# Performance work log

Measured on AMD Instinct MI355X. Metric: run time of the kernel, lower is better.

## Reference

```python
import jax, jax.numpy as jnp
import numpy as np

INV_TEMP = 20.0
THRESHOLD = 0.01
SING_CUTOFF = 3.0
D0 = 128  # order-0 descriptor block
EPS = 1e-6


def setup_inputs() -> dict:
    key = jax.random.key(0)
    ks = jax.random.split(key, 6)
    B, N, M, D = 4, 4096, 4096, 256
    K = (D - D0) // 2
    return {
        "keypoints_A": jax.random.uniform(ks[0], (B, N, 2), jnp.float32) * 2.0 - 1.0,
        "descriptions_A": jax.random.normal(ks[1], (B, N, D), jnp.float32),
        "keypoints_B": jax.random.uniform(ks[2], (B, M, 2), jnp.float32) * 2.0 - 1.0,
        "descriptions_B": jax.random.normal(ks[3], (B, M, D), jnp.float32),
        "W_lstsq": jax.random.normal(ks[4], (D0, K), jnp.float32) * 0.1,
        "b_lstsq": jnp.zeros((K,), jnp.float32),
    }


def _svdvals_2x2(A):
    # singular values of [..,2,2] via eigenvalues of A^T A (closed form)
    M = jnp.einsum('...ki,...kj->...ij', A, A)
    t = M[..., 0, 0] + M[..., 1, 1]
    d = M[..., 0, 0] * M[..., 1, 1] - M[..., 0, 1] * M[..., 1, 0]
    disc = jnp.sqrt(jnp.maximum(0.25 * t * t - d, 0.0))
    lam_hi = 0.5 * t + disc
    lam_lo = jnp.maximum(0.5 * t - disc, 0.0)
    return jnp.sqrt(lam_hi), jnp.sqrt(lam_lo)


def reference(keypoints_A, descriptions_A, keypoints_B, descriptions_B, W_lstsq, b_lstsq):
    B, N, D = descriptions_A.shape
    K = (D - D0) // 2
    # --- dual softmax matcher (normalize=True) ---
    dA = descriptions_A / jnp.linalg.norm(descriptions_A, axis=-1, keepdims=True)
    dB = descriptions_B / jnp.linalg.norm(descriptions_B, axis=-1, keepdims=True)
    sim = INV_TEMP * jnp.einsum('bnd,bmd->bnm', dA, dB)  # [B,N,M]
    P = jax.nn.softmax(sim, axis=-2) * jax.nn.softmax(sim, axis=-1)
    # --- mutual nearest neighbors, fixed-shape (one candidate per A-row) ---
    j = jnp.argmax(P, axis=-1)  # [B,N]
    Pij = jnp.take_along_axis(P, j[..., None], axis=-1)[..., 0]
    colmax_j = jnp.take_along_axis(P.max(axis=-2), j, axis=-1)
    valid = (Pij >= colmax_j) & (Pij > THRESHOLD)  # mutual max + threshold
    # --- gather raw descriptors for matched pairs ---
    descB_m = jnp.take_along_axis(descriptions_B, j[..., None], axis=1)  # [B,N,D]
    desc0_A, desc1_A = descriptions_A[..., :D0], descriptions_A[..., D0:]
    desc0_B, desc1_B = descB_m[..., :D0], descB_m[..., D0:]
    # --- lstsq weights from order-0 features ---
    wA = jax.nn.softplus(desc0_A @ W_lstsq + b_lstsq)
    wB = jax.nn.softplus(desc0_B @ W_lstsq + b_lstsq)
    w = jnp.sqrt(wA * wB)  # [B,N,K]
    # --- weighted 2x2 affine lstsq: A x ~ y ---
    X = desc1_A.reshape(B, N, K, 2)
    Y = desc1_B.reshape(B, N, K, 2)
    G = jnp.einsum('bnk,bnki,bnkj->bnij', w, X, X) + EPS * jnp.eye(2, dtype=X.dtype)
    C = jnp.einsum('bnk,bnki,bnkj->bnij', w, Y, X)
    est = jnp.swapaxes(jnp.linalg.solve(G, jnp.swapaxes(C, -1, -2)), -1, -2)  # [B,N,2,2]
    # --- singular value / determinant filter ---
    s_hi, s_lo = _svdvals_2x2(est)
    good = jnp.isfinite(s_hi + s_lo) & (s_hi < SING_CUTOFF) & (s_lo > 1.0 / SING_CUTOFF)
    det = est[..., 0, 0] * est[..., 1, 1] - est[..., 0, 1] * est[..., 1, 0]
    good = good & (det > 0)  # remove_negative_determinants=True
    valid = valid & good
    matches_A = keypoints_A  # row i of A pairs with column j[b,i]
    matches_B = jnp.take_along_axis(keypoints_B, j[..., None], axis=1)
    return matches_A, matches_B, j, valid
```

## Files before the change

kernel.cpp:

```cpp
#include <hip/hip_runtime.h>
#include <math.h>

#define Bb   4
#define Nn   4096
#define Mm   4096
#define Dd   256
#define D0c  128
#define Kc   64

typedef _Float16 half8 __attribute__((ext_vector_type(8)));
typedef float    f32x4 __attribute__((ext_vector_type(4)));

__device__ __forceinline__ unsigned encf(float f) {
    unsigned u = __float_as_uint(f);
    return (u & 0x80000000u) ? ~u : (u | 0x80000000u);
}
__device__ __forceinline__ float decf(unsigned u) {
    return (u & 0x80000000u) ? __uint_as_float(u ^ 0x80000000u) : __uint_as_float(~u);
}
__device__ __forceinline__ float softplusf(float x) {
    return fmaxf(x, 0.f) + log1pf(expf(-fabsf(x)));
}
__device__ __forceinline__ void gl_lds16(const _Float16* g, _Float16* l) {
    __builtin_amdgcn_global_load_lds((const __attribute__((address_space(1))) void*)g,
                                     (__attribute__((address_space(3))) void*)l, 16, 0, 0);
}

__device__ __forceinline__ void decode_tile(int bid, int swz, int& mt, int& nt, int& zz) {
    if (swz == 2) {
        const int xcd = bid & 7, k = bid >> 3;
        zz = xcd >> 2;
        const int s = xcd & 3;
        mt = (s & 1) * 16 + (k & 15);
        nt = (s >> 1) * 16 + (k >> 4);
    } else if (swz == 1) {
        const int xcd = bid & 7, k = bid >> 3;
        zz = 0;
        const int s = xcd >> 1;
        const int t = (xcd & 1) * 128 + k;
        mt = (s & 1) * 16 + (t & 15);
        nt = (s >> 1) * 16 + (t >> 4);
    } else {
        mt = bid & 31; nt = (bid >> 5) & 31; zz = bid >> 10;
    }
}

__global__ __launch_bounds__(256) void prep_kernel(
    const float* __restrict__ dA, const float* __restrict__ dB,
    _Float16* __restrict__ Ah, _Float16* __restrict__ Al,
    _Float16* __restrict__ Bh, _Float16* __restrict__ Bl,
    unsigned* __restrict__ colMaxU)
{
    const int t = threadIdx.x, wave = t >> 6, lane = t & 63;
    const int row = blockIdx.x * 4 + wave;
    if (blockIdx.y == 0 && lane == 0) colMaxU[row] = 0u;
    const float* src = blockIdx.y ? dB : dA;
    _Float16* dh = blockIdx.y ? Bh : Ah;
    _Float16* dl = blockIdx.y ? Bl : Al;
    const float4 v = *(const float4*)&src[(size_t)row * Dd + lane * 4];
    float ss = v.x * v.x + v.y * v.y + v.z * v.z + v.w * v.w;
#pragma unroll
    for (int m = 32; m; m >>= 1) ss += __shfl_xor(ss, m, 64);
    const float inv = 1.0f / sqrtf(ss);
    float x[4] = {v.x * inv, v.y * inv, v.z * inv, v.w * inv};
    union { _Float16 h[4]; uint2 u; } ph, pl;
#pragma unroll
    for (int i = 0; i < 4; i++) {
        _Float16 h = (_Float16)x[i];
        ph.h[i] = h;
        pl.h[i] = (_Float16)(x[i] - (float)h);
    }
    const size_t toff = (size_t)(row >> 7) * 32768
                      + (size_t)(lane >> 3) * 4096
                      + (size_t)((lane >> 1) & 3) * 1024
                      + (size_t)(row & 127) * 8 + (lane & 1) * 4;
    *(uint2*)&dh[toff] = ph.u;
    *(uint2*)&dl[toff] = pl.u;
}

template<int PB, int STORE>
__global__ __launch_bounds__(256, 3) void sim_kernel(
    const _Float16* __restrict__ Ah, const _Float16* __restrict__ Al,
    const _Float16* __restrict__ Bh, const _Float16* __restrict__ Bl,
    const float* __restrict__ Lrow_g, const float* __restrict__ Lcol_g,
    float* __restrict__ rowsumP, float* __restrict__ colsumP,
    float* __restrict__ rkey, int* __restrict__ rmArr, float* __restrict__ rcvArr,
    unsigned* __restrict__ cmU, float* __restrict__ simG, int b0, int swz)
{
    __shared__ _Float16 lds[4][4][128][8];
    __shared__ float    colp[128];
    __shared__ float    rowp[128];
    __shared__ unsigned colu[128];
    __shared__ float    shL[128], shLc[128];
    __shared__ float    s_bk[128], s_bc[128];
    __shared__ int      s_bm[128];

    const int t = threadIdx.x;
    const int wave = t >> 6, lane = t & 63;
    const int wr = wave >> 1, wc = wave & 1;
    int mt, nt, bbl;
    decode_tile(blockIdx.x, swz, mt, nt, bbl);
    const int bb = b0 + bbl;
    const int n0 = nt * 128, m0 = mt * 128;

    if (PB) {
        if (t < 128) {
            shL[t]  = Lrow_g[bb * Nn + n0 + t];
            shLc[t] = Lcol_g[bb * Mm + m0 + t];
            colu[t] = 0u;
        }
    } else {
        if (t < 128) { colp[t] = 0.f; rowp[t] = 0.f; }
    }

    const _Float16* gb;
    {
        const size_t offA = (size_t)(bb * Nn + n0) * Dd;
        const size_t offB = (size_t)(bb * Mm + m0) * Dd;
        if      (wave == 0) gb = Ah + offA;
        else if (wave == 1) gb = Al + offA;
        else if (wave == 2) gb = Bh + offB;
        else                gb = Bl + offB;
    }

    f32x4 acc[4][4];
#pragma unroll
    for (int ti = 0; ti < 4; ti++)
#pragma unroll
        for (int tj = 0; tj < 4; tj++) acc[ti][tj] = (f32x4)0.f;

    const int quad = lane >> 4, l15 = lane & 15;
    _Float16* ldsw = &lds[wave][0][0][0];

    for (int kc8 = 0; kc8 < 8; ++kc8) {
        const _Float16* gsrc = gb + kc8 * 4096;
#pragma unroll
        for (int q = 0; q < 8; ++q)
            gl_lds16(gsrc + q * 512 + lane * 8, ldsw + q * 512);
        __syncthreads();

        half8 afh[4], afl[4];
#pragma unroll
        for (int ti = 0; ti < 4; ++ti) {
            afh[ti] = *(const half8*)&lds[0][quad][wr * 64 + ti * 16 + l15][0];
            afl[ti] = *(const half8*)&lds[1][quad][wr * 64 + ti * 16 + l15][0];
        }
#pragma unroll
        for (int tj = 0; tj < 4; ++tj) {
            half8 bh = *(const half8*)&lds[2][quad][wc * 64 + tj * 16 + l15][0];
            half8 bl = *(const half8*)&lds[3][quad][wc * 64 + tj * 16 + l15][0];
#pragma unroll
            for (int ti = 0; ti < 4; ++ti) {
                acc[ti][tj] = __builtin_amdgcn_mfma_f32_16x16x32_f16(afh[ti], bh, acc[ti][tj], 0, 0, 0);
                acc[ti][tj] = __builtin_amdgcn_mfma_f32_16x16x32_f16(afh[ti], bl, acc[ti][tj], 0, 0, 0);
                acc[ti][tj] = __builtin_amdgcn_mfma_f32_16x16x32_f16(afl[ti], bh, acc[ti][tj], 0, 0, 0);
            }
        }
        __syncthreads();
    }

    if (!PB) {
        float rp[16] = {0.f}, cp[4] = {0.f};
#pragma unroll
        for (int ti = 0; ti < 4; ++ti)
#pragma unroll
            for (int tj = 0; tj < 4; ++tj)
#pragma unroll
                for (int r = 0; r < 4; ++r) {
                    float e = __expf(fmaf(20.f, acc[ti][tj][r], -20.f));
                    rp[ti * 4 + r] += e;
                    cp[tj] += e;
                }
#pragma unroll
        for (int i = 0; i < 16; ++i)
#pragma unroll
            for (int m = 1; m < 16; m <<= 1) rp[i] += __shfl_xor(rp[i], m, 64);
        if (l15 == 0) {
#pragma unroll
            for (int ti = 0; ti < 4; ++ti)
#pragma unroll
                for (int r = 0; r < 4; ++r)
                    atomicAdd(&rowp[wr * 64 + ti * 16 + quad * 4 + r], rp[ti * 4 + r]);
        }
#pragma unroll
        for (int tj = 0; tj < 4; ++tj) {
            cp[tj] += __shfl_xor(cp[tj], 16, 64);
            cp[tj] += __shfl_xor(cp[tj], 32, 64);
        }
        if (quad == 0) {
#pragma unroll
            for (int tj = 0; tj < 4; ++tj) atomicAdd(&colp[wc * 64 + tj * 16 + l15], cp[tj]);
        }
        __syncthreads();
        if (t < 128) {
            rowsumP[(size_t)(bb * 32 + mt) * Nn + n0 + t] = rowp[t];
            colsumP[(size_t)(bb * 32 + nt) * Mm + m0 + t] = colp[t];
        }
        if (STORE) {
            float* base = simG + ((size_t)bbl * Nn + n0) * Mm + m0 + wc * 64;
#pragma unroll
            for (int ti = 0; ti < 4; ++ti)
#pragma unroll
                for (int r = 0; r < 4; ++r) {
                    float* rowp_ = base + (size_t)(wr * 64 + ti * 16 + quad * 4 + r) * Mm;
#pragma unroll
                    for (int tj = 0; tj < 4; ++tj)
                        __builtin_nontemporal_store(acc[ti][tj][r], rowp_ + tj * 16 + l15);
                }
        }
    } else {
        float Lr[16];
#pragma unroll
        for (int ti = 0; ti < 4; ++ti)
#pragma unroll
            for (int r = 0; r < 4; ++r)
                Lr[ti * 4 + r] = shL[wr * 64 + ti * 16 + quad * 4 + r];

        float bk[16], bc[16];
        int bm[16];
        unsigned cu[4];
#pragma unroll
        for (int i = 0; i < 16; i++) { bk[i] = -INFINITY; bc[i] = -INFINITY; bm[i] = 0x7fffffff; }
#pragma unroll
        for (int j = 0; j < 4; j++) cu[j] = 0u;

#pragma unroll
        for (int ti = 0; ti < 4; ++ti)
#pragma unroll
            for (int tj = 0; tj < 4; ++tj)
#pragma unroll
                for (int r = 0; r < 4; ++r) {
                    float cv = fmaf(40.f, acc[ti][tj][r], -40.f - Lr[ti * 4 + r]);
                    float kv = cv - shLc[wc * 64 + tj * 16 + l15];
                    const int i = ti * 4 + r;
                    if (kv > bk[i]) { bk[i] = kv; bm[i] = m0 + wc * 64 + tj * 16 + l15; bc[i] = cv; }
                    unsigned e = encf(cv);
                    if (e > cu[tj]) cu[tj] = e;
                }
#pragma unroll
        for (int i = 0; i < 16; ++i) {
#pragma unroll
            for (int m = 1; m < 16; m <<= 1) {
                float okv = __shfl_xor(bk[i], m, 64);
                int   om  = __shfl_xor(bm[i], m, 64);
                float ocv = __shfl_xor(bc[i], m, 64);
                if (okv > bk[i] || (okv == bk[i] && om < bm[i])) { bk[i] = okv; bm[i] = om; bc[i] = ocv; }
            }
        }
        if (l15 == 0 && wc == 0) {
#pragma unroll
            for (int ti = 0; ti < 4; ++ti)
#pragma unroll
                for (int r = 0; r < 4; ++r) {
                    const int row = wr * 64 + ti * 16 + quad * 4 + r, i = ti * 4 + r;
                    s_bk[row] = bk[i]; s_bm[row] = bm[i]; s_bc[row] = bc[i];
                }
        }
        __syncthreads();
        if (l15 == 0 && wc == 1) {
#pragma unroll
            for (int ti = 0; ti < 4; ++ti)
#pragma unroll
                for (int r = 0; r < 4; ++r) {
                    const int row = wr * 64 + ti * 16 + quad * 4 + r, i = ti * 4 + r;
                    float k0 = s_bk[row];
                    if (bk[i] > k0 || (bk[i] == k0 && bm[i] < s_bm[row])) {
                        s_bk[row] = bk[i]; s_bm[row] = bm[i]; s_bc[row] = bc[i];
                    }
                }
        }
#pragma unroll
        for (int tj = 0; tj < 4; ++tj) {
            unsigned o = __shfl_xor(cu[tj], 16, 64); if (o > cu[tj]) cu[tj] = o;
            o = __shfl_xor(cu[tj], 32, 64); if (o > cu[tj]) cu[tj] = o;
        }
        if (quad == 0) {
#pragma unroll
            for (int tj = 0; tj < 4; ++tj) atomicMax(&colu[wc * 64 + tj * 16 + l15], cu[tj]);
        }
        __syncthreads();
        if (t < 128) {
            size_t idx = (size_t)(bb * 32 + mt) * Nn + n0 + t;
            rkey[idx] = s_bk[t]; rmArr[idx] = s_bm[t]; rcvArr[idx] = s_bc[t];
            cmU[(size_t)(bb * 32 + nt) * Mm + m0 + t] = colu[t];
        }
    }
}

__global__ __launch_bounds__(256) void logsum_kernel(
    const float* __restrict__ rowsumP, const float* __restrict__ colsumP,
    float* __restrict__ Lrow, float* __restrict__ Lcol, int b0, int CB)
{
    int t = blockIdx.x * 256 + threadIdx.x;
    int half = CB * 4096;
    int which = t >= half;
    int idx = which ? (t - half) : t;
    int bb = b0 + (idx >> 12), n = idx & 4095;
    const float* P = which ? colsumP : rowsumP;
    float s = 0.f;
    for (int mt = 0; mt < 32; ++mt) s += P[(size_t)(bb * 32 + mt) * 4096 + n];
    (which ? Lcol : Lrow)[bb * 4096 + n] = logf(s);
}

__global__ __launch_bounds__(256) void scan_kernel(
    const float* __restrict__ simG,
    const float* __restrict__ Lrow, const float* __restrict__ Lcol,
    float* __restrict__ kvP, float* __restrict__ cvP, int* __restrict__ jP,
    unsigned* __restrict__ colMaxU, int b0)
{
    __shared__ unsigned colu[1024];
    const int t = threadIdx.x, wave = t >> 6, lane = t & 63;
    const int blk = blockIdx.x;
    const int bbl = blk >> 10;
    const int r10 = blk & 1023;
    const int stripe = r10 >> 2, q = r10 & 3;
    const int bb = b0 + bbl;
    const int col0 = q * 1024;
    const int row0 = stripe * 16 + wave * 4;

    for (int i = t; i < 1024; i += 256) colu[i] = 0u;
    __syncthreads();

    f32x4 Lc4[4], cmax[4];
    const float* LcB = Lcol + bb * Mm + col0;
#pragma unroll
    for (int c = 0; c < 4; ++c) {
        Lc4[c] = *(const f32x4*)&LcB[c * 256 + lane * 4];
        cmax[c] = (f32x4)(-INFINITY);
    }

    const float* rowbase = simG + (size_t)(bbl * Nn + row0) * Mm + col0;
    f32x4 cur[4], nxt[4];
#pragma unroll
    for (int c = 0; c < 4; ++c)
        cur[c] = __builtin_nontemporal_load((const f32x4*)&rowbase[c * 256 + lane * 4]);

    for (int r = 0; r < 4; ++r) {
        if (r < 3) {
            const float* nrow = rowbase + (size_t)(r + 1) * Mm;
#pragma unroll
            for (int c = 0; c < 4; ++c)
                nxt[c] = __builtin_nontemporal_load((const f32x4*)&nrow[c * 256 + lane * 4]);
        }
        const int n = bb * Nn + row0 + r;
        const float Ln = Lrow[n];
        const float cbias = -40.f - Ln;
        float bk = -INFINITY, bc = -INFINITY;
        int bm = 0x7fffffff;
#pragma unroll
        for (int c = 0; c < 4; ++c) {
            float cv0 = fmaf(40.f, cur[c].x, cbias);
            float cv1 = fmaf(40.f, cur[c].y, cbias);
            float cv2 = fmaf(40.f, cur[c].z, cbias);
            float cv3 = fmaf(40.f, cur[c].w, cbias);
            cmax[c].x = fmaxf(cmax[c].x, cv0);
            cmax[c].y = fmaxf(cmax[c].y, cv1);
            cmax[c].z = fmaxf(cmax[c].z, cv2);
            cmax[c].w = fmaxf(cmax[c].w, cv3);
            const int mb = col0 + c * 256 + lane * 4;
            float kv0 = cv0 - Lc4[c].x;
            float kv1 = cv1 - Lc4[c].y;
            float kv2 = cv2 - Lc4[c].z;
            float kv3 = cv3 - Lc4[c].w;
            if (kv0 > bk) { bk = kv0; bm = mb;     bc = cv0; }
            if (kv1 > bk) { bk = kv1; bm = mb + 1; bc = cv1; }
            if (kv2 > bk) { bk = kv2; bm = mb + 2; bc = cv2; }
            if (kv3 > bk) { bk = kv3; bm = mb + 3; bc = cv3; }
        }
#pragma unroll
        for (int sh = 1; sh < 64; sh <<= 1) {
            float okv = __shfl_xor(bk, sh, 64);
            int   om  = __shfl_xor(bm, sh, 64);
            float ocv = __shfl_xor(bc, sh, 64);
            if (okv > bk || (okv == bk && om < bm)) { bk = okv; bm = om; bc = ocv; }
        }
        if (lane == 0) {
            size_t o = ((size_t)bb * Nn + row0 + r) * 4 + q;
            kvP[o] = bk; cvP[o] = bc; jP[o] = bm;
        }
#pragma unroll
        for (int c = 0; c < 4; ++c) cur[c] = nxt[c];
    }
#pragma unroll
    for (int c = 0; c < 4; ++c) {
        const int mb = c * 256 + lane * 4;
        atomicMax(&colu[mb],     encf(cmax[c].x));
        atomicMax(&colu[mb + 1], encf(cmax[c].y));
        atomicMax(&colu[mb + 2], encf(cmax[c].z));
        atomicMax(&colu[mb + 3], encf(cmax[c].w));
    }
    __syncthreads();
    unsigned* cm = colMaxU + (size_t)bb * Mm + col0;
    for (int i = t; i < 1024; i += 256) atomicMax(&cm[i], colu[i]);
}

__global__ __launch_bounds__(256) void validate_kernel(
    const float* __restrict__ kvP, const float* __restrict__ cvP,
    const int* __restrict__ jP, const unsigned* __restrict__ colMaxU,
    float* __restrict__ outJ, int* __restrict__ jIdx, int* __restrict__ v1)
{
    const float LOG_THR = -4.605170185988091f;
    const int p = blockIdx.x * 256 + threadIdx.x;
    const int bb = p >> 12;
    float bk = -INFINITY, bc = -INFINITY;
    int bm = 0x7fffffff;
#pragma unroll
    for (int q = 0; q < 4; ++q) {
        size_t o = (size_t)p * 4 + q;
        float k = kvP[o];
        int   m = jP[o];
        if (k > bk || (k == bk && m < bm)) { bk = k; bm = m; bc = cvP[o]; }
    }
    const float cm = decf(colMaxU[(size_t)bb * Mm + bm]);
    const int ok = (bk > LOG_THR) && (bc >= cm);
    outJ[p] = (float)bm;
    jIdx[p] = bm;
    v1[p] = ok;
}

__global__ __launch_bounds__(256) void finalize_kernel(
    const float* __restrict__ rkey, const int* __restrict__ rmArr,
    const float* __restrict__ rcvArr, const unsigned* __restrict__ cmU,
    float* __restrict__ outJ, int* __restrict__ jIdx, int* __restrict__ v1)
{
    const float LOG_THR = -4.605170185988091f;
    int p = blockIdx.x * 256 + threadIdx.x;
    int bb = p >> 12, n = p & 4095;
    float bk = -INFINITY, bc = -INFINITY;
    int bm = 0;
    for (int mt = 0; mt < 32; ++mt) {
        size_t idx = (size_t)(bb * 32 + mt) * Nn + n;
        float k = rkey[idx];
        if (k > bk) { bk = k; bm = rmArr[idx]; bc = rcvArr[idx]; }
    }
    unsigned u = 0u;
    for (int nt = 0; nt < 32; ++nt) {
        unsigned c = cmU[(size_t)(bb * 32 + nt) * Mm + bm];
        if (c > u) u = c;
    }
    float cm = decf(u);
    int ok = (bk > LOG_THR) && (bc >= cm);
    outJ[p] = (float)bm;
    jIdx[p] = bm;
    v1[p]   = ok;
}

__global__ __launch_bounds__(256) void affine_kernel(
    const float* __restrict__ descA, const float* __restrict__ descB,
    const float* __restrict__ kpA, const float* __restrict__ kpB,
    const float* __restrict__ W, const float* __restrict__ bvec,
    const int* __restrict__ jIdx, const int* __restrict__ v1,
    float* __restrict__ outA, float* __restrict__ outB, float* __restrict__ outV)
{
    __shared__ float Ws[D0c * Kc];
    __shared__ float sbuf[4][4][D0c];
    const int t = threadIdx.x, wave = t >> 6, lane = t & 63;
    for (int i = t; i < D0c * Kc; i += 256) Ws[i] = W[i];
    const float bl = bvec[lane];
    __syncthreads();

    float* s0A = sbuf[wave][0];
    float* s1A = sbuf[wave][1];
    float* s0B = sbuf[wave][2];
    float* s1B = sbuf[wave][3];

    for (int p = 0; p < 8; ++p) {
        const int point = blockIdx.x * 32 + wave * 8 + p;
        const int bb = point >> 12;
        const int j = jIdx[point];
        const float* da = descA + (size_t)point * Dd;
        const float* db = descB + (size_t)(bb * Mm + j) * Dd;
        s0A[lane] = da[lane];       s0A[64 + lane] = da[64 + lane];
        s1A[lane] = da[128 + lane]; s1A[64 + lane] = da[192 + lane];
        s0B[lane] = db[lane];       s0B[64 + lane] = db[64 + lane];
        s1B[lane] = db[128 + lane]; s1B[64 + lane] = db[192 + lane];
        __syncthreads();

        float xa = bl, xb = bl;
#pragma unroll 8
        for (int d = 0; d < 128; ++d) {
            float w_ = Ws[d * 64 + lane];
            xa = fmaf(s0A[d], w_, xa);
            xb = fmaf(s0B[d], w_, xb);
        }
        float wa = softplusf(xa), wb = softplusf(xb);
        float w = sqrtf(wa * wb);
        float x0 = s1A[2 * lane], x1 = s1A[2 * lane + 1];
        float y0 = s1B[2 * lane], y1 = s1B[2 * lane + 1];
        float g00 = w * x0 * x0, g01 = w * x0 * x1, g11 = w * x1 * x1;
        float c00 = w * y0 * x0, c01 = w * y0 * x1;
        float c10 = w * y1 * x0, c11 = w * y1 * x1;
#pragma unroll
        for (int m = 32; m; m >>= 1) {
            g00 += __shfl_xor(g00, m, 64); g01 += __shfl_xor(g01, m, 64); g11 += __shfl_xor(g11, m, 64);
            c00 += __shfl_xor(c00, m, 64); c01 += __shfl_xor(c01, m, 64);
            c10 += __shfl_xor(c10, m, 64); c11 += __shfl_xor(c11, m, 64);
        }
        if (lane == 0) {
            g00 += 1e-6f; g11 += 1e-6f;
            float det = g00 * g11 - g01 * g01;
            float e00 = (c00 * g11 - c01 * g01) / det;
            float e01 = (c01 * g00 - c00 * g01) / det;
            float e10 = (c10 * g11 - c11 * g01) / det;
            float e11 = (c11 * g00 - c10 * g01) / det;
            float m00 = e00 * e00 + e10 * e10;
            float m01 = e00 * e01 + e10 * e11;
            float m11 = e01 * e01 + e11 * e11;
            float tr = m00 + m11;
            float dm = m00 * m11 - m01 * m01;
            float disc = sqrtf(fmaxf(0.25f * tr * tr - dm, 0.f));
            float lhi = 0.5f * tr + disc;
            float llo = fmaxf(0.5f * tr - disc, 0.f);
            float shi = sqrtf(lhi), slo = sqrtf(llo);
            float sdet = e00 * e11 - e01 * e10;
            int good = isfinite(shi + slo) && (shi < 3.0f) && (slo > 0.33333334f) && (sdet > 0.f);
            int valid = v1[point] && good;
            outA[2 * point]     = kpA[2 * point];
            outA[2 * point + 1] = kpA[2 * point + 1];
            const float* kb = kpB + (size_t)(bb * Mm + j) * 2;
            outB[2 * point]     = kb[0];
            outB[2 * point + 1] = kb[1];
            outV[point] = valid ? 1.f : 0.f;
        }
        __syncthreads();
    }
}

extern "C" void kernel_launch(void* const* d_in, const int* in_sizes, int n_in,
                              void* d_out, int out_size, void* d_ws, size_t ws_size,
                              hipStream_t stream) {
    const float* kpA = (const float*)d_in[0];
    const float* dA  = (const float*)d_in[1];
    const float* kpB = (const float*)d_in[2];
    const float* dB  = (const float*)d_in[3];
    const float* W   = (const float*)d_in[4];
    const float* bl  = (const float*)d_in[5];
    float* out = (float*)d_out;

    char* ws = (char*)d_ws;
    _Float16* Ah = (_Float16*)ws;  ws += 8388608;
    _Float16* Al = (_Float16*)ws;  ws += 8388608;
    _Float16* Bh = (_Float16*)ws;  ws += 8388608;
    _Float16* Bl = (_Float16*)ws;  ws += 8388608;
    float*    rowsumP = (float*)ws;    ws += 2097152;
    float*    colsumP = (float*)ws;    ws += 2097152;
    float*    Lrow    = (float*)ws;    ws += 65536;
    float*    Lcol    = (float*)ws;    ws += 65536;
    int*      jIdx    = (int*)ws;      ws += 65536;
    int*      v1      = (int*)ws;      ws += 65536;
    float*    kvP     = (float*)ws;    ws += 262144;
    float*    cvP     = (float*)ws;    ws += 262144;
    int*      jP      = (int*)ws;      ws += 262144;
    unsigned* colMaxU = (unsigned*)ws; ws += 65536;
    char*     big     = ws;

    const size_t base = (size_t)(big - (char*)d_ws);

    float*    rkey  = (float*)big;
    int*      rmArr = (int*)(big + 2097152);
    float*    rcvArr= (float*)(big + 4194304);
    unsigned* cmU   = (unsigned*)(big + 6291456);

    float* outA = out;
    float* outB = out + 32768;
    float* outJ = out + 65536;
    float* outV = out + 81920;

    const size_t per = 67108864ull;
    int CB = 0;
    if      (ws_size >= base + 2 * per) CB = 2;
    else if (ws_size >= base + 1 * per) CB = 1;

    prep_kernel<<<dim3(4096, 2), 256, 0, stream>>>(dA, dB, Ah, Al, Bh, Bl, colMaxU);

    if (CB) {
        float* simG = (float*)big;
        for (int b0 = 0; b0 < Bb; b0 += CB) {
            sim_kernel<0, 1><<<1024 * CB, 256, 0, stream>>>(
                Ah, Al, Bh, Bl, nullptr, nullptr, rowsumP, colsumP,
                nullptr, nullptr, nullptr, nullptr, simG, b0, CB);
            logsum_kernel<<<32 * CB, 256, 0, stream>>>(rowsumP, colsumP, Lrow, Lcol, b0, CB);
            scan_kernel<<<1024 * CB, 256, 0, stream>>>(simG, Lrow, Lcol, kvP, cvP, jP, colMaxU, b0);
        }
        validate_kernel<<<64, 256, 0, stream>>>(kvP, cvP, jP, colMaxU, outJ, jIdx, v1);
    } else {
        sim_kernel<0, 0><<<4096, 256, 0, stream>>>(
            Ah, Al, Bh, Bl, nullptr, nullptr, rowsumP, colsumP,
            nullptr, nullptr, nullptr, nullptr, nullptr, 0, 0);
        logsum_kernel<<<32 * Bb, 256, 0, stream>>>(rowsumP, colsumP, Lrow, Lcol, 0, Bb);
        sim_kernel<1, 0><<<4096, 256, 0, stream>>>(
            Ah, Al, Bh, Bl, Lrow, Lcol, nullptr, nullptr,
            rkey, rmArr, rcvArr, cmU, nullptr, 0, 0);
        finalize_kernel<<<64, 256, 0, stream>>>(rkey, rmArr, rcvArr, cmU, outJ, jIdx, v1);
    }
    affine_kernel<<<512, 256, 0, stream>>>(dA, dB, kpA, kpB, W, bl, jIdx, v1, outA, outB, outV);
}
```

Baseline: 304.1 us.

## Fuse previous batch's row/column scan into next batch's similarity GEMM

Replaces the two-batch chunked pipeline with per-batch double-buffered similarity buffers. While computing batch b's similarity tile, two waves of each block scan batch b-1's stored similarity rows, producing row argmax keys and column maxima. Only the last batch gets a standalone scan. The aim is to hide the memory-bound scan behind MFMA work and remove separate scan launches. The cost is extra register pressure and extra load traffic inside the GEMM kernel, plus a dependence on the block-to-stripe mapping.

```diff
diff --git a/kernel.cpp b/kernel.cpp
--- a/kernel.cpp
+++ b/kernel.cpp
@@ -27,13 +27,7 @@
 }
 
 __device__ __forceinline__ void decode_tile(int bid, int swz, int& mt, int& nt, int& zz) {
-    if (swz == 2) {
-        const int xcd = bid & 7, k = bid >> 3;
-        zz = xcd >> 2;
-        const int s = xcd & 3;
-        mt = (s & 1) * 16 + (k & 15);
-        nt = (s >> 1) * 16 + (k >> 4);
-    } else if (swz == 1) {
+    if (swz == 1) {
         const int xcd = bid & 7, k = bid >> 3;
         zz = 0;
         const int s = xcd >> 1;
@@ -78,14 +72,15 @@
     *(uint2*)&dl[toff] = pl.u;
 }
 
-template<int PB, int STORE>
+template<int PB, int STORE, int SCAN>
 __global__ __launch_bounds__(256, 3) void sim_kernel(
     const _Float16* __restrict__ Ah, const _Float16* __restrict__ Al,
     const _Float16* __restrict__ Bh, const _Float16* __restrict__ Bl,
     const float* __restrict__ Lrow_g, const float* __restrict__ Lcol_g,
     float* __restrict__ rowsumP, float* __restrict__ colsumP,
     float* __restrict__ rkey, int* __restrict__ rmArr, float* __restrict__ rcvArr,
-    unsigned* __restrict__ cmU, float* __restrict__ simG, int b0, int swz)
+    unsigned* __restrict__ cmU, float* __restrict__ simG,
+    const float* __restrict__ simPrev, int b0, int swz)
 {
     __shared__ _Float16 lds[4][4][128][8];
     __shared__ float    colp[128];
@@ -94,6 +89,7 @@
     __shared__ float    shL[128], shLc[128];
     __shared__ float    s_bk[128], s_bc[128];
     __shared__ int      s_bm[128];
+    __shared__ float    shLp[16];
 
     const int t = threadIdx.x;
     const int wave = t >> 6, lane = t & 63;
@@ -111,6 +107,21 @@
         }
     } else {
         if (t < 128) { colp[t] = 0.f; rowp[t] = 0.f; }
+    }
+
+    int stripe_s = 0, q_s = 0;
+    f32x4 Lc4s[4], cmaxs[4];
+    if (SCAN) {
+        stripe_s = blockIdx.x >> 2;
+        q_s = blockIdx.x & 3;
+        if (t < 16) shLp[t] = Lrow_g[(size_t)(b0 - 1) * Nn + stripe_s * 16 + t];
+        if (wave < 2) {
+            const float* LcB = Lcol_g + (size_t)(b0 - 1) * Mm + q_s * 1024;
+#pragma unroll
+            for (int c = 0; c < 4; ++c) Lc4s[c] = *(const f32x4*)&LcB[c * 256 + lane * 4];
+        }
+#pragma unroll
+        for (int c = 0; c < 4; ++c) cmaxs[c] = (f32x4)(-INFINITY);
     }
 
     const _Float16* gb;
@@ -133,6 +144,14 @@
     _Float16* ldsw = &lds[wave][0][0][0];
 
     for (int kc8 = 0; kc8 < 8; ++kc8) {
+        f32x4 curs[4];
+        if (SCAN && wave < 2) {
+            const int rr = kc8 * 2 + wave;
+            const float* rp = simPrev + (size_t)(stripe_s * 16 + rr) * Mm + q_s * 1024;
+#pragma unroll
+            for (int c = 0; c < 4; ++c)
+                curs[c] = __builtin_nontemporal_load((const f32x4*)&rp[c * 256 + lane * 4]);
+        }
         const _Float16* gsrc = gb + kc8 * 4096;
 #pragma unroll
         for (int q = 0; q < 8; ++q)
@@ -156,6 +175,44 @@
                 acc[ti][tj] = __builtin_amdgcn_mfma_f32_16x16x32_f16(afl[ti], bh, acc[ti][tj], 0, 0, 0);
             }
         }
+        if (SCAN && wave < 2) {
+            const int rr = kc8 * 2 + wave;
+            const float Ln = shLp[rr];
+            const float cbias = -40.f - Ln;
+            float bk = -INFINITY, bc = -INFINITY;
+            int bm = 0x7fffffff;
+#pragma unroll
+            for (int c = 0; c < 4; ++c) {
+                float cv0 = fmaf(40.f, curs[c].x, cbias);
+                float cv1 = fmaf(40.f, curs[c].y, cbias);
+                float cv2 = fmaf(40.f, curs[c].z, cbias);
+                float cv3 = fmaf(40.f, curs[c].w, cbias);
+                cmaxs[c].x = fmaxf(cmaxs[c].x, cv0);
+                cmaxs[c].y = fmaxf(cmaxs[c].y, cv1);
+                cmaxs[c].z = fmaxf(cmaxs[c].z, cv2);
+                cmaxs[c].w = fmaxf(cmaxs[c].w, cv3);
+                const int mb = q_s * 1024 + c * 256 + lane * 4;
+                float kv0 = cv0 - Lc4s[c].x;
+                float kv1 = cv1 - Lc4s[c].y;
+                float kv2 = cv2 - Lc4s[c].z;
+                float kv3 = cv3 - Lc4s[c].w;
+                if (kv0 > bk) { bk = kv0; bm = mb;     bc = cv0; }
+                if (kv1 > bk) { bk = kv1; bm = mb + 1; bc = cv1; }
+                if (kv2 > bk) { bk = kv2; bm = mb + 2; bc = cv2; }
+                if (kv3 > bk) { bk = kv3; bm = mb + 3; bc = cv3; }
+            }
+#pragma unroll
+            for (int sh = 1; sh < 64; sh <<= 1) {
+                float okv = __shfl_xor(bk, sh, 64);
+                int   om  = __shfl_xor(bm, sh, 64);
+                float ocv = __shfl_xor(bc, sh, 64);
+                if (okv > bk || (okv == bk && om < bm)) { bk = okv; bm = om; bc = ocv; }
+            }
+            if (lane == 0) {
+                size_t o = ((size_t)(b0 - 1) * Nn + stripe_s * 16 + rr) * 4 + q_s;
+                rkey[o] = bk; rcvArr[o] = bc; rmArr[o] = bm;
+            }
+        }
         __syncthreads();
     }
 
@@ -207,6 +264,25 @@
                     for (int tj = 0; tj < 4; ++tj)
                         __builtin_nontemporal_store(acc[ti][tj][r], rowp_ + tj * 16 + l15);
                 }
+        }
+        if (SCAN) {
+            unsigned* colu2 = (unsigned*)&lds[0][0][0][0];
+            __syncthreads();
+            for (int i = t; i < 1024; i += 256) colu2[i] = 0u;
+            __syncthreads();
+            if (wave < 2) {
+#pragma unroll
+                for (int c = 0; c < 4; ++c) {
+                    const int mb = c * 256 + lane * 4;
+                    atomicMax(&colu2[mb],     encf(cmaxs[c].x));
+                    atomicMax(&colu2[mb + 1], encf(cmaxs[c].y));
+                    atomicMax(&colu2[mb + 2], encf(cmaxs[c].z));
+                    atomicMax(&colu2[mb + 3], encf(cmaxs[c].w));
+                }
+            }
+            __syncthreads();
+            unsigned* cm = cmU + (size_t)(b0 - 1) * Mm + q_s * 1024;
+            for (int i = t; i < 1024; i += 256) atomicMax(&cm[i], colu2[i]);
         }
     } else {
         float Lr[16];
@@ -311,10 +387,8 @@
     __shared__ unsigned colu[1024];
     const int t = threadIdx.x, wave = t >> 6, lane = t & 63;
     const int blk = blockIdx.x;
-    const int bbl = blk >> 10;
-    const int r10 = blk & 1023;
-    const int stripe = r10 >> 2, q = r10 & 3;
-    const int bb = b0 + bbl;
+    const int stripe = blk >> 2, q = blk & 3;
+    const int bb = b0;
     const int col0 = q * 1024;
     const int row0 = stripe * 16 + wave * 4;
 
@@ -322,14 +396,14 @@
     __syncthreads();
 
     f32x4 Lc4[4], cmax[4];
-    const float* LcB = Lcol + bb * Mm + col0;
+    const float* LcB = Lcol + (size_t)bb * Mm + col0;
 #pragma unroll
     for (int c = 0; c < 4; ++c) {
         Lc4[c] = *(const f32x4*)&LcB[c * 256 + lane * 4];
         cmax[c] = (f32x4)(-INFINITY);
     }
 
-    const float* rowbase = simG + (size_t)(bbl * Nn + row0) * Mm + col0;
+    const float* rowbase = simG + (size_t)row0 * Mm + col0;
     f32x4 cur[4], nxt[4];
 #pragma unroll
     for (int c = 0; c < 4; ++c)
@@ -342,8 +416,7 @@
             for (int c = 0; c < 4; ++c)
                 nxt[c] = __builtin_nontemporal_load((const f32x4*)&nrow[c * 256 + lane * 4]);
         }
-        const int n = bb * Nn + row0 + r;
-        const float Ln = Lrow[n];
+        const float Ln = Lrow[(size_t)bb * Nn + row0 + r];
         const float cbias = -40.f - Ln;
         float bk = -INFINITY, bc = -INFINITY;
         int bm = 0x7fffffff;
@@ -567,30 +640,36 @@
     float* outV = out + 81920;
 
     const size_t per = 67108864ull;
-    int CB = 0;
-    if      (ws_size >= base + 2 * per) CB = 2;
-    else if (ws_size >= base + 1 * per) CB = 1;
+    const int havebuf = (ws_size >= base + 2 * per);
 
     prep_kernel<<<dim3(4096, 2), 256, 0, stream>>>(dA, dB, Ah, Al, Bh, Bl, colMaxU);
 
-    if (CB) {
-        float* simG = (float*)big;
-        for (int b0 = 0; b0 < Bb; b0 += CB) {
-            sim_kernel<0, 1><<<1024 * CB, 256, 0, stream>>>(
-                Ah, Al, Bh, Bl, nullptr, nullptr, rowsumP, colsumP,
-                nullptr, nullptr, nullptr, nullptr, simG, b0, CB);
-            logsum_kernel<<<32 * CB, 256, 0, stream>>>(rowsumP, colsumP, Lrow, Lcol, b0, CB);
-            scan_kernel<<<1024 * CB, 256, 0, stream>>>(simG, Lrow, Lcol, kvP, cvP, jP, colMaxU, b0);
-        }
+    if (havebuf) {
+        float* buf0 = (float*)big;
+        float* buf1 = (float*)(big + per);
+        for (int bb = 0; bb < Bb; ++bb) {
+            float*       cur  = (bb & 1) ? buf1 : buf0;
+            const float* prev = (bb & 1) ? buf0 : buf1;
+            if (bb == 0)
+                sim_kernel<0, 1, 0><<<1024, 256, 0, stream>>>(
+                    Ah, Al, Bh, Bl, nullptr, nullptr, rowsumP, colsumP,
+                    nullptr, nullptr, nullptr, nullptr, cur, nullptr, bb, 1);
+            else
+                sim_kernel<0, 1, 1><<<1024, 256, 0, stream>>>(
+                    Ah, Al, Bh, Bl, Lrow, Lcol, rowsumP, colsumP,
+                    kvP, jP, cvP, colMaxU, cur, prev, bb, 1);
+            logsum_kernel<<<32, 256, 0, stream>>>(rowsumP, colsumP, Lrow, Lcol, bb, 1);
+        }
+        scan_kernel<<<1024, 256, 0, stream>>>(buf1, Lrow, Lcol, kvP, cvP, jP, colMaxU, 3);
         validate_kernel<<<64, 256, 0, stream>>>(kvP, cvP, jP, colMaxU, outJ, jIdx, v1);
     } else {
-        sim_kernel<0, 0><<<4096, 256, 0, stream>>>(
+        sim_kernel<0, 0, 0><<<4096, 256, 0, stream>>>(
             Ah, Al, Bh, Bl, nullptr, nullptr, rowsumP, colsumP,
-            nullptr, nullptr, nullptr, nullptr, nullptr, 0, 0);
+            nullptr, nullptr, nullptr, nullptr, nullptr, nullptr, 0, 0);
         logsum_kernel<<<32 * Bb, 256, 0, stream>>>(rowsumP, colsumP, Lrow, Lcol, 0, Bb);
-        sim_kernel<1, 0><<<4096, 256, 0, stream>>>(
+        sim_kernel<1, 0, 0><<<4096, 256, 0, stream>>>(
             Ah, Al, Bh, Bl, Lrow, Lcol, nullptr, nullptr,
-            rkey, rmArr, rcvArr, cmU, nullptr, 0, 0);
+            rkey, rmArr, rcvArr, cmU, nullptr, nullptr, 0, 0);
         finalize_kernel<<<64, 256, 0, stream>>>(rkey, rmArr, rcvArr, cmU, outJ, jIdx, v1);
     }
     affine_kernel<<<512, 256, 0, stream>>>(dA, dB, kpA, kpB, W, bl, jIdx, v1, outA, outB, outV);
```

Result: slower. 451.9 us (+48.6%).

## Enlarge sim tile to 256x128 with 512-thread blocks sharing B tile

Applied to the files above, without the earlier changes.

Doubles the row tile of the similarity GEMM to 256 A rows per block using 8 waves, so each loaded B tile is reused by twice as many rows. This cuts global/LDS load traffic per output. LDS is unified into one buffer and reused for reduction scratch. The XCD swizzle mapping and the partial-sum arrays (colsum and col-max) are re-indexed for 16 row tiles. Risks: larger LDS footprint and a new launch bound of 6 may reduce occupancy, and the unchanged STORE path may not cover the 256-row tile.

```diff
diff --git a/kernel.cpp b/kernel.cpp
--- a/kernel.cpp
+++ b/kernel.cpp
@@ -29,19 +29,17 @@
 __device__ __forceinline__ void decode_tile(int bid, int swz, int& mt, int& nt, int& zz) {
     if (swz == 2) {
         const int xcd = bid & 7, k = bid >> 3;
-        zz = xcd >> 2;
-        const int s = xcd & 3;
-        mt = (s & 1) * 16 + (k & 15);
-        nt = (s >> 1) * 16 + (k >> 4);
+        zz = k >> 6;
+        const int kk = k & 63;
+        mt = (xcd & 3) * 8 + (kk & 7);
+        nt = (xcd >> 2) * 8 + (kk >> 3);
     } else if (swz == 1) {
         const int xcd = bid & 7, k = bid >> 3;
         zz = 0;
-        const int s = xcd >> 1;
-        const int t = (xcd & 1) * 128 + k;
-        mt = (s & 1) * 16 + (t & 15);
-        nt = (s >> 1) * 16 + (t >> 4);
+        mt = (xcd & 3) * 8 + (k & 7);
+        nt = (xcd >> 2) * 8 + (k >> 3);
     } else {
-        mt = bid & 31; nt = (bid >> 5) & 31; zz = bid >> 10;
+        mt = bid & 31; nt = (bid >> 5) & 15; zz = bid >> 9;
     }
 }
 
@@ -79,7 +77,7 @@
 }
 
 template<int PB, int STORE>
-__global__ __launch_bounds__(256, 3) void sim_kernel(
+__global__ __launch_bounds__(512, 6) void sim_kernel(
     const _Float16* __restrict__ Ah, const _Float16* __restrict__ Al,
     const _Float16* __restrict__ Bh, const _Float16* __restrict__ Bl,
     const float* __restrict__ Lrow_g, const float* __restrict__ Lcol_g,
@@ -87,41 +85,21 @@
     float* __restrict__ rkey, int* __restrict__ rmArr, float* __restrict__ rcvArr,
     unsigned* __restrict__ cmU, float* __restrict__ simG, int b0, int swz)
 {
-    __shared__ _Float16 lds[4][4][128][8];
-    __shared__ float    colp[128];
-    __shared__ float    rowp[128];
-    __shared__ unsigned colu[128];
-    __shared__ float    shL[128], shLc[128];
-    __shared__ float    s_bk[128], s_bc[128];
-    __shared__ int      s_bm[128];
+    __shared__ _Float16 S[24576];
 
     const int t = threadIdx.x;
     const int wave = t >> 6, lane = t & 63;
     const int wr = wave >> 1, wc = wave & 1;
+    const int quad = lane >> 4, l15 = lane & 15;
     int mt, nt, bbl;
     decode_tile(blockIdx.x, swz, mt, nt, bbl);
     const int bb = b0 + bbl;
-    const int n0 = nt * 128, m0 = mt * 128;
-
-    if (PB) {
-        if (t < 128) {
-            shL[t]  = Lrow_g[bb * Nn + n0 + t];
-            shLc[t] = Lcol_g[bb * Mm + m0 + t];
-            colu[t] = 0u;
-        }
-    } else {
-        if (t < 128) { colp[t] = 0.f; rowp[t] = 0.f; }
-    }
-
-    const _Float16* gb;
-    {
-        const size_t offA = (size_t)(bb * Nn + n0) * Dd;
-        const size_t offB = (size_t)(bb * Mm + m0) * Dd;
-        if      (wave == 0) gb = Ah + offA;
-        else if (wave == 1) gb = Al + offA;
-        else if (wave == 2) gb = Bh + offB;
-        else                gb = Bl + offB;
-    }
+    const int n0 = nt * 256, m0 = mt * 128;
+
+    const _Float16* gAh = Ah + (size_t)(bb * 32 + nt * 2) * 32768;
+    const _Float16* gAl = Al + (size_t)(bb * 32 + nt * 2) * 32768;
+    const _Float16* gBh = Bh + (size_t)(bb * 32 + mt) * 32768;
+    const _Float16* gBl = Bl + (size_t)(bb * 32 + mt) * 32768;
 
     f32x4 acc[4][4];
 #pragma unroll
@@ -129,26 +107,41 @@
 #pragma unroll
         for (int tj = 0; tj < 4; tj++) acc[ti][tj] = (f32x4)0.f;
 
-    const int quad = lane >> 4, l15 = lane & 15;
-    _Float16* ldsw = &lds[wave][0][0][0];
+    const int grpA = wr >> 1;
+    const int arl = (wr & 1) * 64;
 
     for (int kc8 = 0; kc8 < 8; ++kc8) {
-        const _Float16* gsrc = gb + kc8 * 4096;
-#pragma unroll
-        for (int q = 0; q < 8; ++q)
-            gl_lds16(gsrc + q * 512 + lane * 8, ldsw + q * 512);
+#pragma unroll
+        for (int q = 0; q < 6; ++q) {
+            const int c = wave * 6 + q;
+            _Float16* dst = S + c * 512;
+            const _Float16* src;
+            if (c < 32) {
+                const int ca = c & 15;
+                const _Float16* gA = (c < 16) ? gAh : gAl;
+                src = gA + ((ca >> 1) & 1) * 32768 + kc8 * 4096
+                        + (ca >> 2) * 1024 + (ca & 1) * 512;
+            } else {
+                const int cb = c & 7;
+                const _Float16* gB = (c < 40) ? gBh : gBl;
+                src = gB + kc8 * 4096 + (cb >> 1) * 1024 + (cb & 1) * 512;
+            }
+            gl_lds16(src + lane * 8, dst);
+        }
         __syncthreads();
 
         half8 afh[4], afl[4];
 #pragma unroll
         for (int ti = 0; ti < 4; ++ti) {
-            afh[ti] = *(const half8*)&lds[0][quad][wr * 64 + ti * 16 + l15][0];
-            afl[ti] = *(const half8*)&lds[1][quad][wr * 64 + ti * 16 + l15][0];
+            const int r8 = (arl + ti * 16 + l15) * 8;
+            afh[ti] = *(const half8*)&S[        quad * 2048 + grpA * 1024 + r8];
+            afl[ti] = *(const half8*)&S[8192 + quad * 2048 + grpA * 1024 + r8];
         }
 #pragma unroll
         for (int tj = 0; tj < 4; ++tj) {
-            half8 bh = *(const half8*)&lds[2][quad][wc * 64 + tj * 16 + l15][0];
-            half8 bl = *(const half8*)&lds[3][quad][wc * 64 + tj * 16 + l15][0];
+            const int c8 = (wc * 64 + tj * 16 + l15) * 8;
+            half8 bh = *(const half8*)&S[16384 + quad * 1024 + c8];
+            half8 bl = *(const half8*)&S[20480 + quad * 1024 + c8];
 #pragma unroll
             for (int ti = 0; ti < 4; ++ti) {
                 acc[ti][tj] = __builtin_amdgcn_mfma_f32_16x16x32_f16(afh[ti], bh, acc[ti][tj], 0, 0, 0);
@@ -160,7 +153,15 @@
     }
 
     if (!PB) {
-        float rp[16] = {0.f}, cp[4] = {0.f};
+        float* rowpS = (float*)S;
+        float* colpS = (float*)S + 256;
+        if (t < 256) rowpS[t] = 0.f;
+        if (t < 128) colpS[t] = 0.f;
+        __syncthreads();
+
+        float rp[16], cp[4] = {0.f, 0.f, 0.f, 0.f};
+#pragma unroll
+        for (int i = 0; i < 16; ++i) rp[i] = 0.f;
 #pragma unroll
         for (int ti = 0; ti < 4; ++ti)
 #pragma unroll
@@ -180,7 +181,7 @@
             for (int ti = 0; ti < 4; ++ti)
 #pragma unroll
                 for (int r = 0; r < 4; ++r)
-                    atomicAdd(&rowp[wr * 64 + ti * 16 + quad * 4 + r], rp[ti * 4 + r]);
+                    atomicAdd(&rowpS[wr * 64 + ti * 16 + quad * 4 + r], rp[ti * 4 + r]);
         }
 #pragma unroll
         for (int tj = 0; tj < 4; ++tj) {
@@ -189,13 +190,11 @@
         }
         if (quad == 0) {
 #pragma unroll
-            for (int tj = 0; tj < 4; ++tj) atomicAdd(&colp[wc * 64 + tj * 16 + l15], cp[tj]);
-        }
-        __syncthreads();
-        if (t < 128) {
-            rowsumP[(size_t)(bb * 32 + mt) * Nn + n0 + t] = rowp[t];
-            colsumP[(size_t)(bb * 32 + nt) * Mm + m0 + t] = colp[t];
-        }
+            for (int tj = 0; tj < 4; ++tj) atomicAdd(&colpS[wc * 64 + tj * 16 + l15], cp[tj]);
+        }
+        __syncthreads();
+        if (t < 256) rowsumP[(size_t)(bb * 32 + mt) * Nn + n0 + t] = rowpS[t];
+        if (t < 128) colsumP[(size_t)(bb * 16 + nt) * Mm + m0 + t] = colpS[t];
         if (STORE) {
             float* base = simG + ((size_t)bbl * Nn + n0) * Mm + m0 + wc * 64;
 #pragma unroll
@@ -209,6 +208,16 @@
                 }
         }
     } else {
+        float*    shL  = (float*)S;
+        float*    shLc = (float*)S + 256;
+        float*    s_bk = (float*)S + 384;
+        float*    s_bc = (float*)S + 640;
+        int*      s_bm = (int*)((float*)S + 896);
+        unsigned* colu = (unsigned*)((float*)S + 1152);
+        if (t < 256) shL[t] = Lrow_g[bb * Nn + n0 + t];
+        if (t < 128) { shLc[t] = Lcol_g[bb * Mm + m0 + t]; colu[t] = 0u; }
+        __syncthreads();
+
         float Lr[16];
 #pragma unroll
         for (int ti = 0; ti < 4; ++ti)
@@ -256,6 +265,15 @@
                     s_bk[row] = bk[i]; s_bm[row] = bm[i]; s_bc[row] = bc[i];
                 }
         }
+#pragma unroll
+        for (int tj = 0; tj < 4; ++tj) {
+            unsigned o = __shfl_xor(cu[tj], 16, 64); if (o > cu[tj]) cu[tj] = o;
+            o = __shfl_xor(cu[tj], 32, 64); if (o > cu[tj]) cu[tj] = o;
+        }
+        if (quad == 0) {
+#pragma unroll
+            for (int tj = 0; tj < 4; ++tj) atomicMax(&colu[wc * 64 + tj * 16 + l15], cu[tj]);
+        }
         __syncthreads();
         if (l15 == 0 && wc == 1) {
 #pragma unroll
@@ -269,21 +287,12 @@
                     }
                 }
         }
-#pragma unroll
-        for (int tj = 0; tj < 4; ++tj) {
-            unsigned o = __shfl_xor(cu[tj], 16, 64); if (o > cu[tj]) cu[tj] = o;
-            o = __shfl_xor(cu[tj], 32, 64); if (o > cu[tj]) cu[tj] = o;
-        }
-        if (quad == 0) {
-#pragma unroll
-            for (int tj = 0; tj < 4; ++tj) atomicMax(&colu[wc * 64 + tj * 16 + l15], cu[tj]);
-        }
-        __syncthreads();
-        if (t < 128) {
+        __syncthreads();
+        if (t < 256) {
             size_t idx = (size_t)(bb * 32 + mt) * Nn + n0 + t;
             rkey[idx] = s_bk[t]; rmArr[idx] = s_bm[t]; rcvArr[idx] = s_bc[t];
-            cmU[(size_t)(bb * 32 + nt) * Mm + m0 + t] = colu[t];
-        }
+        }
+        if (t < 128) cmU[(size_t)(bb * 16 + nt) * Mm + m0 + t] = colu[t];
     }
 }
 
@@ -296,10 +305,14 @@
     int which = t >= half;
     int idx = which ? (t - half) : t;
     int bb = b0 + (idx >> 12), n = idx & 4095;
-    const float* P = which ? colsumP : rowsumP;
     float s = 0.f;
-    for (int mt = 0; mt < 32; ++mt) s += P[(size_t)(bb * 32 + mt) * 4096 + n];
-    (which ? Lcol : Lrow)[bb * 4096 + n] = logf(s);
+    if (which) {
+        for (int nt = 0; nt < 16; ++nt) s += colsumP[(size_t)(bb * 16 + nt) * 4096 + n];
+        Lcol[bb * 4096 + n] = logf(s);
+    } else {
+        for (int mt = 0; mt < 32; ++mt) s += rowsumP[(size_t)(bb * 32 + mt) * 4096 + n];
+        Lrow[bb * 4096 + n] = logf(s);
+    }
 }
 
 __global__ __launch_bounds__(256) void scan_kernel(
@@ -434,8 +447,8 @@
         if (k > bk) { bk = k; bm = rmArr[idx]; bc = rcvArr[idx]; }
     }
     unsigned u = 0u;
-    for (int nt = 0; nt < 32; ++nt) {
-        unsigned c = cmU[(size_t)(bb * 32 + nt) * Mm + bm];
+    for (int nt = 0; nt < 16; ++nt) {
+        unsigned c = cmU[(size_t)(bb * 16 + nt) * Mm + bm];
         if (c > u) u = c;
     }
     float cm = decf(u);
@@ -576,7 +589,7 @@
     if (CB) {
         float* simG = (float*)big;
         for (int b0 = 0; b0 < Bb; b0 += CB) {
-            sim_kernel<0, 1><<<1024 * CB, 256, 0, stream>>>(
+            sim_kernel<0, 1><<<512 * CB, 512, 0, stream>>>(
                 Ah, Al, Bh, Bl, nullptr, nullptr, rowsumP, colsumP,
                 nullptr, nullptr, nullptr, nullptr, simG, b0, CB);
             logsum_kernel<<<32 * CB, 256, 0, stream>>>(rowsumP, colsumP, Lrow, Lcol, b0, CB);
@@ -584,11 +597,11 @@
         }
         validate_kernel<<<64, 256, 0, stream>>>(kvP, cvP, jP, colMaxU, outJ, jIdx, v1);
     } else {
-        sim_kernel<0, 0><<<4096, 256, 0, stream>>>(
+        sim_kernel<0, 0><<<512 * Bb, 512, 0, stream>>>(
             Ah, Al, Bh, Bl, nullptr, nullptr, rowsumP, colsumP,
             nullptr, nullptr, nullptr, nullptr, nullptr, 0, 0);
         logsum_kernel<<<32 * Bb, 256, 0, stream>>>(rowsumP, colsumP, Lrow, Lcol, 0, Bb);
-        sim_kernel<1, 0><<<4096, 256, 0, stream>>>(
+        sim_kernel<1, 0><<<512 * Bb, 512, 0, stream>>>(
             Ah, Al, Bh, Bl, Lrow, Lcol, nullptr, nullptr,
             rkey, rmArr, rcvArr, cmU, nullptr, 0, 0);
         finalize_kernel<<<64, 256, 0, stream>>>(rkey, rmArr, rcvArr, cmU, outJ, jIdx, v1);
```

After: 1.029 ms. +238.6%, slower.
